# Optimization experiments

Hardware: AMD Instinct MI355X
Metric: run time of the kernel (lower is better)

The kernel has to match this reference:

```python
import jax, jax.numpy as jnp
import numpy as np

EPS = 1e-6


def setup_inputs() -> dict:
    key = jax.random.key(0)
    k1, k2 = jax.random.split(key)
    S, B, H, F = 4096, 8, 1024, 1024
    x = jax.random.normal(k1, (S, B, H), dtype=jnp.float32)
    scale = jnp.ones((H,), dtype=jnp.float32)
    ln_bias = jnp.zeros((H,), dtype=jnp.float32)
    # variance_scaling(1.0, 'fan_in', 'truncated_normal') ~ normal with std 1/sqrt(fan_in)
    kernel = jax.random.normal(k2, (H, F), dtype=jnp.float32) * (1.0 / np.sqrt(H))
    return {"x": x, "scale": scale, "ln_bias": ln_bias, "kernel": kernel}


def reference(x, scale, ln_bias, kernel):
    # LayerNorm over last (hidden) axis; zero_centered_gamma=False:
    #   y = (x - mean) / sqrt(var + eps) * gamma + beta
    mu = jnp.mean(x, axis=-1, keepdims=True)
    var = jnp.mean(jnp.square(x - mu), axis=-1, keepdims=True)
    ln_out = (x - mu) * jax.lax.rsqrt(var + EPS) * scale + ln_bias
    # DenseGeneral: contract hidden axis with kernel (H, F); use_bias=False, no depth scaling
    out = jnp.einsum("sbh,hf->sbf", ln_out, kernel)
    # return_layernorm_output=True -> (out, ln_out)
    return (out, ln_out)
```

## Files before the change

kernel.cpp:

```cpp
#include <hip/hip_runtime.h>
#include <stdint.h>

typedef unsigned short u16;

#define S_ 4096
#define B_ 8
#define H_ 1024
#define F_ 1024
#define M_ (S_ * B_)
#define N_ F_
#define K_ H_

#define BM 128
#define BN 128
#define BK 64

typedef short short8 __attribute__((ext_vector_type(8)));
typedef float floatx4 __attribute__((ext_vector_type(4)));

__device__ __forceinline__ u16 f2bf(float f) {
    union { float f; uint32_t u; } c;
    c.f = f;
    uint32_t u = c.u;
    uint32_t r = (u + 0x7fffu + ((u >> 16) & 1u)) >> 16;
    return (u16)r;
}

__device__ __forceinline__ void async_load16(const void* gptr, void* lptr) {
    __builtin_amdgcn_global_load_lds(
        (const __attribute__((address_space(1))) uint32_t*)gptr,
        (__attribute__((address_space(3))) uint32_t*)lptr,
        16 , 0 , 0 );
}

__global__ __launch_bounds__(256) void transpose_cast_kernel(
    const float* __restrict__ w, u16* __restrict__ bt)
{
    __shared__ float tile[32][33];
    const int tx = threadIdx.x;
    const int ty = threadIdx.y;
    const int n0 = blockIdx.x * 32;
    const int k0 = blockIdx.y * 32;
#pragma unroll
    for (int j = 0; j < 4; ++j)
        tile[ty + j * 8][tx] = w[(size_t)(k0 + ty + j * 8) * N_ + n0 + tx];
    __syncthreads();
#pragma unroll
    for (int j = 0; j < 4; ++j)
        bt[(size_t)(n0 + ty + j * 8) * K_ + k0 + tx] =
            f2bf(tile[tx][ty + j * 8]);
}

__global__ __launch_bounds__(256) void ln_kernel(
    const float* __restrict__ x, const float* __restrict__ scale,
    const float* __restrict__ bias, float* __restrict__ ln_out,
    u16* __restrict__ ln_bf16)
{
    const int row = blockIdx.x;
    const int tid = threadIdx.x;
    const float4 v = reinterpret_cast<const float4*>(x + (size_t)row * H_)[tid];

    float s  = v.x + v.y + v.z + v.w;
    float sq = v.x * v.x + v.y * v.y + v.z * v.z + v.w * v.w;
#pragma unroll
    for (int off = 32; off >= 1; off >>= 1) {
        s  += __shfl_down(s, off, 64);
        sq += __shfl_down(sq, off, 64);
    }
    __shared__ float red[8];
    const int wave = tid >> 6, lane = tid & 63;
    if (lane == 0) { red[wave] = s; red[4 + wave] = sq; }
    __syncthreads();
    const float Ssum = red[0] + red[1] + red[2] + red[3];
    const float Qsum = red[4] + red[5] + red[6] + red[7];
    const float mu   = Ssum * (1.0f / H_);
    const float var  = Qsum * (1.0f / H_) - mu * mu;
    const float rstd = rsqrtf(var + 1e-6f);

    const float4 sc = reinterpret_cast<const float4*>(scale)[tid];
    const float4 bi = reinterpret_cast<const float4*>(bias)[tid];
    float4 y;
    y.x = (v.x - mu) * rstd * sc.x + bi.x;
    y.y = (v.y - mu) * rstd * sc.y + bi.y;
    y.z = (v.z - mu) * rstd * sc.z + bi.z;
    y.w = (v.w - mu) * rstd * sc.w + bi.w;

    reinterpret_cast<float4*>(ln_out + (size_t)row * H_)[tid] = y;

    ushort4 h;
    h.x = f2bf(y.x); h.y = f2bf(y.y); h.z = f2bf(y.z); h.w = f2bf(y.w);
    reinterpret_cast<ushort4*>(ln_bf16 + (size_t)row * H_)[tid] = h;
}

__global__ __launch_bounds__(256) void gemm_bt_kernel(
    const u16* __restrict__ A, const u16* __restrict__ Bt,
    float* __restrict__ C)
{
    __shared__ __align__(16) u16 As[BM * BK];
    __shared__ __align__(16) u16 Bs[BN * BK];

    const int tid  = threadIdx.x;
    const int wave = tid >> 6;
    const int lane = tid & 63;
    const int wm   = wave >> 1;
    const int wn   = wave & 1;

    const int bid  = blockIdx.x;
    const int bx   = (bid >> 3) & 7;
    const int by   = ((bid >> 6) << 3) | (bid & 7);
    const int row0 = by * BM;
    const int col0 = bx * BN;

    floatx4 acc[4][4];
#pragma unroll
    for (int i = 0; i < 4; ++i)
#pragma unroll
        for (int j = 0; j < 4; ++j) acc[i][j] = (floatx4)0.0f;

    const int srow = wave * 8 + (lane >> 3);
    const int scol = (((lane & 7) ^ (lane >> 3)) * 8);
    const u16* Ag = A + (size_t)(row0 + srow) * K_ + scol;
    const u16* Bg = Bt + (size_t)(col0 + srow) * K_ + scol;
    char* AsBase = (char*)As + (size_t)(wave * 8) * (BK * 2);
    char* BsBase = (char*)Bs + (size_t)(wave * 8) * (BK * 2);

    for (int kt = 0; kt < K_ / BK; ++kt) {
        const int k0 = kt * BK;
#pragma unroll
        for (int i = 0; i < 4; ++i) {
            async_load16(Ag + (size_t)(i * 32) * K_ + k0,
                         AsBase + (size_t)(i * 32) * (BK * 2));
            async_load16(Bg + (size_t)(i * 32) * K_ + k0,
                         BsBase + (size_t)(i * 32) * (BK * 2));
        }
        __syncthreads();

#pragma unroll
        for (int ks = 0; ks < 2; ++ks) {
            short8 af[4], bf[4];
#pragma unroll
            for (int mt = 0; mt < 4; ++mt) {
                const int r = wm * 64 + mt * 16 + (lane & 15);
                const int q = ks * 4 + (lane >> 4);
                const int c = q ^ (r & 7);
                af[mt] = *reinterpret_cast<const short8*>(
                    (const char*)As + (size_t)r * (BK * 2) + c * 16);
            }
#pragma unroll
            for (int nt = 0; nt < 4; ++nt) {
                const int r = wn * 64 + nt * 16 + (lane & 15);
                const int q = ks * 4 + (lane >> 4);
                const int c = q ^ (r & 7);
                bf[nt] = *reinterpret_cast<const short8*>(
                    (const char*)Bs + (size_t)r * (BK * 2) + c * 16);
            }
#pragma unroll
            for (int mt = 0; mt < 4; ++mt)
#pragma unroll
                for (int nt = 0; nt < 4; ++nt)
                    acc[mt][nt] = __builtin_amdgcn_mfma_f32_16x16x32_bf16(
                        af[mt], bf[nt], acc[mt][nt], 0, 0, 0);
        }
        __syncthreads();
    }

#pragma unroll
    for (int mt = 0; mt < 4; ++mt) {
#pragma unroll
        for (int nt = 0; nt < 4; ++nt) {
            const int r0 = row0 + wm * 64 + mt * 16 + (lane >> 4) * 4;
            const int c  = col0 + wn * 64 + nt * 16 + (lane & 15);
#pragma unroll
            for (int r = 0; r < 4; ++r)
                C[(size_t)(r0 + r) * N_ + c] = acc[mt][nt][r];
        }
    }
}

extern "C" void kernel_launch(void* const* d_in, const int* in_sizes, int n_in,
                              void* d_out, int out_size, void* d_ws, size_t ws_size,
                              hipStream_t stream) {
    const float* x      = (const float*)d_in[0];
    const float* scale  = (const float*)d_in[1];
    const float* lnbias = (const float*)d_in[2];
    const float* weight = (const float*)d_in[3];

    float* out    = (float*)d_out;
    float* ln_out = (float*)d_out + (size_t)M_ * N_;

    u16* ln_bf16 = (u16*)d_ws;
    u16* bt      = (u16*)d_ws + (size_t)M_ * K_;

    transpose_cast_kernel<<<dim3(N_ / 32, K_ / 32), dim3(32, 8), 0, stream>>>(
        weight, bt);
    ln_kernel<<<M_, 256, 0, stream>>>(x, scale, lnbias, ln_out, ln_bf16);
    gemm_bt_kernel<<<(M_ / BM) * (N_ / BN), 256, 0, stream>>>(ln_bf16, bt, out);
}
```

Measured before the change: 429.1 us.

## Double-buffer larger GEMM tiles and use wave-per-row persistent LayerNorm

The GEMM moves to 256x256 tiles with 512 threads, double-buffered LDS stages loaded asynchronously two k-steps ahead, and raised wave priority around the MFMA bursts. This is meant to overlap global loads with compute and improve operand reuse. The LayerNorm kernel now gives one wave per row in a grid-stride loop with scale and bias held in registers, which removes the block barrier and shared-memory reduction. The larger tiles raise register and LDS pressure (128 KB LDS per block) and leave fewer blocks for wave scheduling.

```diff
diff --git a/kernel.cpp b/kernel.cpp
--- a/kernel.cpp
+++ b/kernel.cpp
@@ -11,9 +11,10 @@
 #define N_ F_
 #define K_ H_
 
-#define BM 128
-#define BN 128
+#define BM 256
+#define BN 256
 #define BK 64
+#define NT (K_ / BK)
 
 typedef short short8 __attribute__((ext_vector_type(8)));
 typedef float floatx4 __attribute__((ext_vector_type(4)));
@@ -51,125 +52,161 @@
             f2bf(tile[tx][ty + j * 8]);
 }
 
+#define LN_BLOCKS 2048
 __global__ __launch_bounds__(256) void ln_kernel(
     const float* __restrict__ x, const float* __restrict__ scale,
     const float* __restrict__ bias, float* __restrict__ ln_out,
     u16* __restrict__ ln_bf16)
 {
-    const int row = blockIdx.x;
-    const int tid = threadIdx.x;
-    const float4 v = reinterpret_cast<const float4*>(x + (size_t)row * H_)[tid];
-
-    float s  = v.x + v.y + v.z + v.w;
-    float sq = v.x * v.x + v.y * v.y + v.z * v.z + v.w * v.w;
-#pragma unroll
-    for (int off = 32; off >= 1; off >>= 1) {
-        s  += __shfl_down(s, off, 64);
-        sq += __shfl_down(sq, off, 64);
-    }
-    __shared__ float red[8];
-    const int wave = tid >> 6, lane = tid & 63;
-    if (lane == 0) { red[wave] = s; red[4 + wave] = sq; }
-    __syncthreads();
-    const float Ssum = red[0] + red[1] + red[2] + red[3];
-    const float Qsum = red[4] + red[5] + red[6] + red[7];
-    const float mu   = Ssum * (1.0f / H_);
-    const float var  = Qsum * (1.0f / H_) - mu * mu;
-    const float rstd = rsqrtf(var + 1e-6f);
-
-    const float4 sc = reinterpret_cast<const float4*>(scale)[tid];
-    const float4 bi = reinterpret_cast<const float4*>(bias)[tid];
-    float4 y;
-    y.x = (v.x - mu) * rstd * sc.x + bi.x;
-    y.y = (v.y - mu) * rstd * sc.y + bi.y;
-    y.z = (v.z - mu) * rstd * sc.z + bi.z;
-    y.w = (v.w - mu) * rstd * sc.w + bi.w;
-
-    reinterpret_cast<float4*>(ln_out + (size_t)row * H_)[tid] = y;
-
-    ushort4 h;
-    h.x = f2bf(y.x); h.y = f2bf(y.y); h.z = f2bf(y.z); h.w = f2bf(y.w);
-    reinterpret_cast<ushort4*>(ln_bf16 + (size_t)row * H_)[tid] = h;
-}
-
-__global__ __launch_bounds__(256) void gemm_bt_kernel(
+    const int lane = threadIdx.x & 63;
+    const int wid  = (blockIdx.x << 2) | (threadIdx.x >> 6);
+    const int nwaves = LN_BLOCKS * 4;
+
+    float4 sc[4], bi[4];
+#pragma unroll
+    for (int j = 0; j < 4; ++j) {
+        sc[j] = reinterpret_cast<const float4*>(scale)[j * 64 + lane];
+        bi[j] = reinterpret_cast<const float4*>(bias)[j * 64 + lane];
+    }
+
+    for (int row = wid; row < M_; row += nwaves) {
+        const float4* xr = reinterpret_cast<const float4*>(x + (size_t)row * H_);
+        float4 v[4];
+        float s = 0.f, sq = 0.f;
+#pragma unroll
+        for (int j = 0; j < 4; ++j) {
+            v[j] = xr[j * 64 + lane];
+            s  += v[j].x + v[j].y + v[j].z + v[j].w;
+            sq += v[j].x * v[j].x + v[j].y * v[j].y +
+                  v[j].z * v[j].z + v[j].w * v[j].w;
+        }
+#pragma unroll
+        for (int off = 32; off >= 1; off >>= 1) {
+            s  += __shfl_xor(s, off, 64);
+            sq += __shfl_xor(sq, off, 64);
+        }
+        const float mu   = s * (1.0f / H_);
+        const float var  = sq * (1.0f / H_) - mu * mu;
+        const float rstd = rsqrtf(var + 1e-6f);
+
+        float4* yr = reinterpret_cast<float4*>(ln_out + (size_t)row * H_);
+        ushort4* hr = reinterpret_cast<ushort4*>(ln_bf16 + (size_t)row * H_);
+#pragma unroll
+        for (int j = 0; j < 4; ++j) {
+            float4 y;
+            y.x = (v[j].x - mu) * rstd * sc[j].x + bi[j].x;
+            y.y = (v[j].y - mu) * rstd * sc[j].y + bi[j].y;
+            y.z = (v[j].z - mu) * rstd * sc[j].z + bi[j].z;
+            y.w = (v[j].w - mu) * rstd * sc[j].w + bi[j].w;
+            yr[j * 64 + lane] = y;
+            ushort4 h;
+            h.x = f2bf(y.x); h.y = f2bf(y.y); h.z = f2bf(y.z); h.w = f2bf(y.w);
+            hr[j * 64 + lane] = h;
+        }
+    }
+}
+
+__global__ __launch_bounds__(512, 2) void gemm_bt_kernel(
     const u16* __restrict__ A, const u16* __restrict__ Bt,
     float* __restrict__ C)
 {
-    __shared__ __align__(16) u16 As[BM * BK];
-    __shared__ __align__(16) u16 Bs[BN * BK];
+    __shared__ __align__(16) u16 As[2][BM * BK];
+    __shared__ __align__(16) u16 Bs[2][BN * BK];
 
     const int tid  = threadIdx.x;
-    const int wave = tid >> 6;
+    const int wid  = tid >> 6;
     const int lane = tid & 63;
-    const int wm   = wave >> 1;
-    const int wn   = wave & 1;
+    const int wm   = wid >> 2;
+    const int wn   = wid & 3;
 
     const int bid  = blockIdx.x;
-    const int bx   = (bid >> 3) & 7;
-    const int by   = ((bid >> 6) << 3) | (bid & 7);
+    const int bx   = (bid >> 3) & 3;
+    const int by   = ((bid >> 5) << 3) | (bid & 7);
     const int row0 = by * BM;
     const int col0 = bx * BN;
 
-    floatx4 acc[4][4];
-#pragma unroll
-    for (int i = 0; i < 4; ++i)
+    floatx4 acc[8][4];
+#pragma unroll
+    for (int i = 0; i < 8; ++i)
 #pragma unroll
         for (int j = 0; j < 4; ++j) acc[i][j] = (floatx4)0.0f;
 
-    const int srow = wave * 8 + (lane >> 3);
-    const int scol = (((lane & 7) ^ (lane >> 3)) * 8);
-    const u16* Ag = A + (size_t)(row0 + srow) * K_ + scol;
-    const u16* Bg = Bt + (size_t)(col0 + srow) * K_ + scol;
-    char* AsBase = (char*)As + (size_t)(wave * 8) * (BK * 2);
-    char* BsBase = (char*)Bs + (size_t)(wave * 8) * (BK * 2);
-
-    for (int kt = 0; kt < K_ / BK; ++kt) {
-        const int k0 = kt * BK;
-#pragma unroll
-        for (int i = 0; i < 4; ++i) {
-            async_load16(Ag + (size_t)(i * 32) * K_ + k0,
-                         AsBase + (size_t)(i * 32) * (BK * 2));
-            async_load16(Bg + (size_t)(i * 32) * K_ + k0,
-                         BsBase + (size_t)(i * 32) * (BK * 2));
-        }
-        __syncthreads();
-
-#pragma unroll
-        for (int ks = 0; ks < 2; ++ks) {
-            short8 af[4], bf[4];
-#pragma unroll
-            for (int mt = 0; mt < 4; ++mt) {
-                const int r = wm * 64 + mt * 16 + (lane & 15);
-                const int q = ks * 4 + (lane >> 4);
-                const int c = q ^ (r & 7);
-                af[mt] = *reinterpret_cast<const short8*>(
-                    (const char*)As + (size_t)r * (BK * 2) + c * 16);
+    const int srow   = (wid << 3) | (lane >> 3);
+    const int schunk = (lane & 7) ^ (srow & 7);
+    const u16* Ag = A  + (size_t)(row0 + srow) * K_ + schunk * 8;
+    const u16* Bg = Bt + (size_t)(col0 + srow) * K_ + schunk * 8;
+
+#define STAGE(buf, kt) do {                                                   \
+    const size_t koff_ = (size_t)(kt) * BK;                                   \
+    _Pragma("unroll")                                                         \
+    for (int i_ = 0; i_ < 4; ++i_) {                                          \
+        async_load16(Ag + (size_t)(i_ * 64) * K_ + koff_,                     \
+                     (char*)As[buf] + (size_t)(i_ * 64 + (wid << 3)) * 128);  \
+        async_load16(Bg + (size_t)(i_ * 64) * K_ + koff_,                     \
+                     (char*)Bs[buf] + (size_t)(i_ * 64 + (wid << 3)) * 128);  \
+    }                                                                         \
+} while (0)
+
+    STAGE(0, 0);
+    STAGE(1, 1);
+    asm volatile("s_waitcnt vmcnt(8)" ::: "memory");
+    __builtin_amdgcn_s_barrier();
+
+    int cur = 0;
+    for (int t = 0; t < NT; ++t) {
+        short8 bfrag[4][2];
+#pragma unroll
+        for (int nt = 0; nt < 4; ++nt)
+#pragma unroll
+            for (int ks = 0; ks < 2; ++ks) {
+                const int r  = (wn << 6) | (nt << 4) | (lane & 15);
+                const int q  = (ks << 2) | (lane >> 4);
+                const int cc = q ^ (r & 7);
+                bfrag[nt][ks] = *reinterpret_cast<const short8*>(
+                    (const char*)Bs[cur] + (size_t)r * 128 + cc * 16);
             }
 #pragma unroll
-            for (int nt = 0; nt < 4; ++nt) {
-                const int r = wn * 64 + nt * 16 + (lane & 15);
-                const int q = ks * 4 + (lane >> 4);
-                const int c = q ^ (r & 7);
-                bf[nt] = *reinterpret_cast<const short8*>(
-                    (const char*)Bs + (size_t)r * (BK * 2) + c * 16);
-            }
-#pragma unroll
-            for (int mt = 0; mt < 4; ++mt)
+        for (int mp = 0; mp < 4; ++mp) {
+            short8 afrag[2][2];
+#pragma unroll
+            for (int mi = 0; mi < 2; ++mi)
+#pragma unroll
+                for (int ks = 0; ks < 2; ++ks) {
+                    const int mt = mp * 2 + mi;
+                    const int r  = (wm << 7) | (mt << 4) | (lane & 15);
+                    const int q  = (ks << 2) | (lane >> 4);
+                    const int cc = q ^ (r & 7);
+                    afrag[mi][ks] = *reinterpret_cast<const short8*>(
+                        (const char*)As[cur] + (size_t)r * 128 + cc * 16);
+                }
+            __builtin_amdgcn_s_setprio(1);
+#pragma unroll
+            for (int mi = 0; mi < 2; ++mi)
 #pragma unroll
                 for (int nt = 0; nt < 4; ++nt)
-                    acc[mt][nt] = __builtin_amdgcn_mfma_f32_16x16x32_bf16(
-                        af[mt], bf[nt], acc[mt][nt], 0, 0, 0);
-        }
-        __syncthreads();
-    }
-
-#pragma unroll
-    for (int mt = 0; mt < 4; ++mt) {
+#pragma unroll
+                    for (int ks = 0; ks < 2; ++ks)
+                        acc[mp * 2 + mi][nt] =
+                            __builtin_amdgcn_mfma_f32_16x16x32_bf16(
+                                afrag[mi][ks], bfrag[nt][ks],
+                                acc[mp * 2 + mi][nt], 0, 0, 0);
+            __builtin_amdgcn_s_setprio(0);
+        }
+
+        if (t == NT - 1) break;
+        asm volatile("s_waitcnt vmcnt(0) lgkmcnt(0)" ::: "memory");
+        __builtin_amdgcn_s_barrier();
+        if (t + 2 < NT) STAGE(cur, t + 2);
+        cur ^= 1;
+    }
+#undef STAGE
+
+#pragma unroll
+    for (int mt = 0; mt < 8; ++mt) {
 #pragma unroll
         for (int nt = 0; nt < 4; ++nt) {
-            const int r0 = row0 + wm * 64 + mt * 16 + (lane >> 4) * 4;
-            const int c  = col0 + wn * 64 + nt * 16 + (lane & 15);
+            const int r0 = row0 + (wm << 7) + (mt << 4) + ((lane >> 4) << 2);
+            const int c  = col0 + (wn << 6) + (nt << 4) + (lane & 15);
 #pragma unroll
             for (int r = 0; r < 4; ++r)
                 C[(size_t)(r0 + r) * N_ + c] = acc[mt][nt][r];
@@ -193,6 +230,6 @@
 
     transpose_cast_kernel<<<dim3(N_ / 32, K_ / 32), dim3(32, 8), 0, stream>>>(
         weight, bt);
-    ln_kernel<<<M_, 256, 0, stream>>>(x, scale, lnbias, ln_out, ln_bf16);
-    gemm_bt_kernel<<<(M_ / BM) * (N_ / BN), 256, 0, stream>>>(ln_bf16, bt, out);
-}
+    ln_kernel<<<LN_BLOCKS, 256, 0, stream>>>(x, scale, lnbias, ln_out, ln_bf16);
+    gemm_bt_kernel<<<(M_ / BM) * (N_ / BN), 512, 0, stream>>>(ln_bf16, bt, out);
+}
```

New measurement: 451.5 us. 1.05x slower.
